# Optimization experiments

Hardware: AMD Instinct MI355X
Metric: run time of the kernel (lower is better)

## Reference

```python
import jax, jax.numpy as jnp
import numpy as np

BLANK = 36
NEG = -1e30  # stand-in for -inf that stays NaN-free under logaddexp


def _ctc_loss(logits, targets, input_lengths, target_lengths):
    """CTC loss (reduction='mean', matching torch.nn.CTCLoss semantics:
    per-sample loss divided by target_length, then mean over batch).
    logits: [B, T, C] raw scores; targets: [B*L] flattened labels (fixed L per sample).
    """
    B, T, C = logits.shape
    L = targets.shape[0] // B
    tgt = targets.reshape(B, L)
    S = 2 * L + 1  # extended label length: blank-interleaved

    # log_softmax over classes, then time-major [T, B, C]
    lp = jnp.transpose(jax.nn.log_softmax(logits, axis=-1), (1, 0, 2))

    # extended targets: [blank, t1, blank, t2, ..., blank]  -> [B, S]
    ext = jnp.full((B, S), BLANK, dtype=tgt.dtype).at[:, 1::2].set(tgt)

    # gather log-probs of extended labels: [T, B, S]
    lp_ext = lp[:, jnp.arange(B)[:, None], ext]

    # positions beyond 2*target_len are invalid
    valid = jnp.arange(S)[None, :] < (2 * target_lengths[:, None] + 1)  # [B, S]
    # skip transition s-2 -> s allowed only if ext[s] != blank and ext[s] != ext[s-2]
    skip_ok = (ext != BLANK) & jnp.concatenate(
        [jnp.zeros((B, 2), bool), ext[:, 2:] != ext[:, :-2]], axis=1)

    end_idx = 2 * target_lengths  # index of final blank; [B]

    def final_ll(alpha):
        e1 = jnp.take_along_axis(alpha, end_idx[:, None], axis=1)[:, 0]
        e2 = jnp.take_along_axis(alpha, (end_idx - 1)[:, None], axis=1)[:, 0]
        return jnp.logaddexp(e1, e2)

    # t = 0 initialization
    alpha0 = jnp.full((B, S), NEG, logits.dtype)
    alpha0 = alpha0.at[:, 0].set(lp_ext[0, :, 0]).at[:, 1].set(lp_ext[0, :, 1])
    alpha0 = jnp.where(valid, alpha0, NEG)
    final0 = jnp.where(input_lengths == 1, final_ll(alpha0), NEG)

    pad1 = jnp.full((B, 1), NEG, logits.dtype)
    pad2 = jnp.full((B, 2), NEG, logits.dtype)

    def step(carry, inp):
        alpha, final = carry
        t, lpe = inp  # lpe: [B, S]
        a1 = jnp.concatenate([pad1, alpha[:, :-1]], axis=1)
        a2 = jnp.where(skip_ok, jnp.concatenate([pad2, alpha[:, :-2]], axis=1), NEG)
        new = jnp.logaddexp(jnp.logaddexp(alpha, a1), a2) + lpe
        new = jnp.where(valid, new, NEG)
        final = jnp.where(input_lengths == t + 1, final_ll(new), final)
        return (new, final), None

    (_, final), _ = jax.lax.scan(step, (alpha0, final0),
                                 (jnp.arange(1, T), lp_ext[1:]))
    return jnp.mean(-final / target_lengths.astype(logits.dtype))


def setup_inputs() -> dict:
    key = jax.random.key(0)
    k1, k2 = jax.random.split(key)
    B, T, C, L = 2048, 256, 37, 16
    logits = jax.random.normal(k1, (B, T, C), dtype=jnp.float32)
    targets = jax.random.randint(k2, (B * L,), 0, 36, dtype=jnp.int32)  # never blank
    input_lengths = jnp.full((B,), T, dtype=jnp.int32)
    target_lengths = jnp.full((B,), L, dtype=jnp.int32)
    return {"logits": logits, "targets": targets,
            "input_lengths": input_lengths, "target_lengths": target_lengths}


def reference(logits, targets, input_lengths, target_lengths):
    return _ctc_loss(logits, targets, input_lengths, target_lengths)
```

## Files before the change

kernel.cpp:

```cpp
#include <hip/hip_runtime.h>

#define BLANK 36
#define NEG -1e30f
#define CC 37
#define LOG37 3.6109179126442243f

__device__ __forceinline__ float logaddexp_f(float a, float b) {
    float m = fmaxf(a, b);
    float d = fabsf(a - b);
    return m + __logf(1.0f + __expf(-d));
}

#define DPP0(src, ctrl) __builtin_amdgcn_update_dpp(0, (src), (ctrl), 0xf, 0xf, true)
#define DPPM(old, src, ctrl) __builtin_amdgcn_update_dpp((old), (src), (ctrl), 0xf, 0xf, false)

__global__ __launch_bounds__(128) void ctc_fused_dpp16_kernel(
    const float* __restrict__ logits,
    const int*   __restrict__ targets,
    const int*   __restrict__ input_lengths,
    const int*   __restrict__ target_lengths,
    float*       __restrict__ per_sample,
    int B, int T, int L)
{
    __shared__ float lds[2 * 4736];
    const int lane = threadIdx.x & 63;
    const int wib  = threadIdx.x >> 6;
    const int b    = blockIdx.x * 2 + wib;
    if (b >= B) return;

    float* X0 = lds + wib * 4736;
    float* X1 = X0 + 2368;

    const int S = 2 * L + 1;
    const int tlen_s = __builtin_amdgcn_readfirstlane(target_lengths[b]);
    const int ilen_s = __builtin_amdgcn_readfirstlane(input_lengths[b]);
    const int end_s  = 2 * tlen_s;

    int ext_s = BLANK;
    if (lane < S && (lane & 1)) ext_s = targets[b * L + (lane >> 1)];
    const int es2 = __shfl_up(ext_s, 2);
    const bool skip_ok = (lane < S) && (lane >= 2) && (ext_s != BLANK) && (ext_s != es2);
    const float kf = skip_ok ? 1.0f : 0.0f;
    const bool valid = lane < (2 * tlen_s + 1);
    const float validm = valid ? 1.0f : 0.0f;

    const bool c16 = ((lane & 31) == 16);
    const bool c17 = ((lane & 31) == 17);
    const bool c32 = (lane == 32);
    const bool c33 = (lane == 33);

    const float4* src = (const float4*)(logits + (size_t)b * T * CC);

    float z = 0.0f, racc = 0.0f, capv = NEG;

    auto STEP = [&](float p, int tt) {
        const int zi  = __float_as_int(z);
        const int s1  = DPP0(zi, 0x111);
        const int s2  = DPP0(zi, 0x112);
        const int b15 = DPP0(zi, 0x142);
        const int b31 = DPP0(zi, 0x143);
        const int y15 = DPP0(s1, 0x142);
        const int y31 = DPP0(s1, 0x143);
        const float a1 = __int_as_float(c16 ? b15 : (c32 ? b31 : s1));
        const float a2 = __int_as_float(c16 ? y15 : (c17 ? b15 : (c32 ? y31 : (c33 ? b31 : s2))));
        z = fmaf(kf, a2, z + a1) * p;
        if (ilen_s == tt + 1)
            capv = __logf(fmaxf(z, 1e-35f)) + racc - (float)(tt + 1) * LOG37;
    };

    auto RESCALE = [&]() {
        float m = z;
        m = fmaxf(m, __int_as_float(DPPM(__float_as_int(m), __float_as_int(m), 0x111)));
        m = fmaxf(m, __int_as_float(DPPM(__float_as_int(m), __float_as_int(m), 0x112)));
        m = fmaxf(m, __int_as_float(DPPM(__float_as_int(m), __float_as_int(m), 0x114)));
        m = fmaxf(m, __int_as_float(DPPM(__float_as_int(m), __float_as_int(m), 0x118)));
        m = fmaxf(m, __int_as_float(DPPM(__float_as_int(m), __float_as_int(m), 0x142)));
        m = fmaxf(m, __int_as_float(DPPM(__float_as_int(m), __float_as_int(m), 0x143)));
        float gm = __int_as_float(__builtin_amdgcn_readlane(__float_as_int(m), 63));
        gm = fmaxf(gm, 1e-30f);
        z *= (1.0f / gm);
        racc += __logf(gm);
    };

    auto SOFTMAX = [&](float* Xn) {
        float xr[CC];
        const float* row = Xn + lane * CC;
        #pragma unroll
        for (int c2 = 0; c2 < CC; ++c2) xr[c2] = row[c2];
        float m = xr[0];
        #pragma unroll
        for (int c2 = 1; c2 < CC; ++c2) m = fmaxf(m, xr[c2]);
        float ss = 0.0f;
        #pragma unroll
        for (int c2 = 0; c2 < CC; ++c2) { xr[c2] = __expf(xr[c2] - m); ss += xr[c2]; }
        const float inv = 37.0f / ss;
        float* wrow = Xn + lane * CC;
        #pragma unroll
        for (int c2 = 0; c2 < CC; ++c2) wrow[c2] = xr[c2] * inv;
    };

    {
        float4* dst = (float4*)X0;
        #pragma unroll
        for (int k = 0; k < 9; ++k) dst[k * 64 + lane] = src[k * 64 + lane];
        if (lane < 16) dst[576 + lane] = src[576 + lane];
        __builtin_amdgcn_s_waitcnt(0);
        SOFTMAX(X0);
        __builtin_amdgcn_s_waitcnt(0);
    }

    const int NC = T >> 6;
    float pw[16];
    #pragma unroll 1
    for (int c = 0; c < NC; ++c) {
        const float* Xb = (c & 1) ? X1 : X0;
        const bool more = (c + 1 < NC);
        const bool first = (c == 0);
        const int tbase = c << 6;

        float4 f0 = {}, f1 = {}, f2 = {}, f3 = {}, f4 = {},
               f5 = {}, f6 = {}, f7 = {}, f8 = {}, f9 = {};
        if (more) {
            const float4* s2g = src + (size_t)(c + 1) * 592;
            f0 = s2g[lane];       f1 = s2g[64 + lane];  f2 = s2g[128 + lane];
            f3 = s2g[192 + lane]; f4 = s2g[256 + lane]; f5 = s2g[320 + lane];
            f6 = s2g[384 + lane]; f7 = s2g[448 + lane]; f8 = s2g[512 + lane];
            if (lane < 16) f9 = s2g[576 + lane];
        }

        #pragma unroll
        for (int j = 0; j < 16; ++j) pw[j] = Xb[j * CC + ext_s];
        #pragma unroll
        for (int r = 0; r < 64; ++r) {
            const float p = pw[r & 15];
            if (r + 16 < 64) pw[r & 15] = Xb[(r + 16) * CC + ext_s];
            if (r == 0) {
                if (first) {
                    z = ((lane <= 1) ? p : 0.0f) * validm;
                    if (ilen_s == 1) capv = __logf(fmaxf(z, 1e-35f)) - LOG37;
                } else {
                    STEP(p, tbase);
                }
            } else {
                STEP(p, tbase + r);
            }
            if ((r & 15) == 15) RESCALE();
        }

        if (more) {
            float* Xn = (c & 1) ? X0 : X1;
            float4* dst = (float4*)Xn;
            dst[lane] = f0;       dst[64 + lane] = f1;  dst[128 + lane] = f2;
            dst[192 + lane] = f3; dst[256 + lane] = f4; dst[320 + lane] = f5;
            dst[384 + lane] = f6; dst[448 + lane] = f7; dst[512 + lane] = f8;
            if (lane < 16) dst[576 + lane] = f9;
            __builtin_amdgcn_s_waitcnt(0);
            SOFTMAX(Xn);
            __builtin_amdgcn_s_waitcnt(0);
        }
    }

    const float e1 = __shfl(capv, end_s);
    const float e2 = __shfl(capv, end_s - 1);
    const float final_v = logaddexp_f(e1, e2);
    if (lane == 0) per_sample[b] = -final_v / (float)tlen_s;
}

__global__ __launch_bounds__(256) void lse_kernel(
    const float* __restrict__ logits, float* __restrict__ denom, int N)
{
    __shared__ float lds[256 * CC];
    const int lane = threadIdx.x & 63;
    const int wib  = threadIdx.x >> 6;
    const int wave = blockIdx.x * 4 + wib;
    const long long row0 = (long long)wave * 64;
    if (row0 >= N) return;
    const int wbase = wib * 64 * CC;
    const float4* src4 = (const float4*)(logits + row0 * CC);
    const long long n4_remaining = ((long long)N * CC - row0 * CC) / 4;
    float4* lds4 = (float4*)(lds + wbase);
    #pragma unroll
    for (int k = 0; k < 10; ++k) {
        const int idx = k * 64 + lane;
        if (idx < 592 && idx < n4_remaining) lds4[idx] = src4[idx];
    }
    __builtin_amdgcn_s_waitcnt(0);
    const long long row = row0 + lane;
    if (row >= N) return;
    const float* x = lds + wbase + lane * CC;
    float m = x[0];
    #pragma unroll
    for (int c = 1; c < CC; ++c) m = fmaxf(m, x[c]);
    float s = 0.0f;
    #pragma unroll
    for (int c = 0; c < CC; ++c) s += __expf(x[c] - m);
    denom[row] = m + __logf(s);
}

__global__ __launch_bounds__(256) void ctc_alpha2_kernel(
    const float* __restrict__ logits, const float* __restrict__ denom,
    const int* __restrict__ targets, const int* __restrict__ input_lengths,
    const int* __restrict__ target_lengths, float* __restrict__ per_sample,
    int B, int T, int L)
{
    const int wave = (int)((blockIdx.x * blockDim.x + threadIdx.x) >> 6);
    const int lane = threadIdx.x & 63;
    if (wave >= B) return;
    const int b = wave;
    const int S = 2 * L + 1;
    const int tlen = target_lengths[b];
    const int ilen = input_lengths[b];
    const int end_idx = 2 * tlen;
    int ext_s = BLANK;
    if (lane < S && (lane & 1)) ext_s = targets[b * L + (lane >> 1)];
    const int ext_sm2 = __shfl_up(ext_s, 2);
    const bool skip_ok = (lane < S) && (lane >= 2) && (ext_s != BLANK) && (ext_s != ext_sm2);
    const bool valid = lane < (2 * tlen + 1);
    const float* lg = logits + (size_t)b * T * CC;
    const float* dn = denom + (size_t)b * T;
    float x_cur = lg[ext_s];
    float d_cur = dn[0];
    float x_nx = (T > 1) ? lg[CC + ext_s] : 0.0f;
    float d_nx = (T > 1) ? dn[1] : 0.0f;
    float final_v = NEG;
    float alpha = (valid && lane <= 1) ? (x_cur - d_cur) : NEG;
    if (ilen == 1) {
        const float e1 = __shfl(alpha, end_idx);
        const float e2 = __shfl(alpha, end_idx - 1);
        final_v = logaddexp_f(e1, e2);
    }
    for (int tt = 1; tt < T; ++tt) {
        x_cur = x_nx; d_cur = d_nx;
        if (tt + 1 < T) {
            x_nx = lg[(size_t)(tt + 1) * CC + ext_s];
            d_nx = dn[tt + 1];
        }
        const float lpe = x_cur - d_cur;
        float a1 = __shfl_up(alpha, 1);
        if (lane == 0) a1 = NEG;
        float a2 = __shfl_up(alpha, 2);
        if (!skip_ok) a2 = NEG;
        const float m = fmaxf(fmaxf(alpha, a1), a2);
        const float s = __expf(alpha - m) + __expf(a1 - m) + __expf(a2 - m);
        const float na = m + __logf(s) + lpe;
        alpha = valid ? na : NEG;
        if (ilen == tt + 1) {
            const float e1 = __shfl(alpha, end_idx);
            const float e2 = __shfl(alpha, end_idx - 1);
            final_v = logaddexp_f(e1, e2);
        }
    }
    if (lane == 0) per_sample[b] = -final_v / (float)tlen;
}

__global__ __launch_bounds__(256) void ctc_alpha_mono_kernel(
    const float* __restrict__ logits, const int* __restrict__ targets,
    const int* __restrict__ input_lengths, const int* __restrict__ target_lengths,
    float* __restrict__ per_sample, int B, int T, int L)
{
    const int wave = (int)((blockIdx.x * blockDim.x + threadIdx.x) >> 6);
    const int lane = threadIdx.x & 63;
    if (wave >= B) return;
    const int b = wave;
    const int S = 2 * L + 1;
    const int tlen = target_lengths[b];
    const int ilen = input_lengths[b];
    const int end_idx = 2 * tlen;
    int ext_s = BLANK;
    if (lane < S && (lane & 1)) ext_s = targets[b * L + (lane >> 1)];
    const int ext_sm2 = __shfl_up(ext_s, 2);
    const bool skip_ok = (lane < S) && (lane >= 2) && (ext_s != BLANK) && (ext_s != ext_sm2);
    const bool valid = lane < (2 * tlen + 1);
    const float* lg = logits + (size_t)b * T * CC;
    float alpha = NEG, final_v = NEG;
    for (int t = 0; t < T; ++t) {
        float x = (lane < CC) ? lg[t * CC + lane] : -3.0e38f;
        float mx = x;
        #pragma unroll
        for (int o = 32; o > 0; o >>= 1) mx = fmaxf(mx, __shfl_xor(mx, o));
        float e = (lane < CC) ? __expf(x - mx) : 0.0f;
        float se = e;
        #pragma unroll
        for (int o = 32; o > 0; o >>= 1) se += __shfl_xor(se, o);
        const float lp = x - mx - __logf(se);
        const float lpe = __shfl(lp, ext_s);
        float newa;
        if (t == 0) {
            newa = (lane <= 1) ? lpe : NEG;
        } else {
            float a1 = __shfl_up(alpha, 1);
            if (lane == 0) a1 = NEG;
            float a2 = __shfl_up(alpha, 2);
            if (!skip_ok) a2 = NEG;
            newa = logaddexp_f(logaddexp_f(alpha, a1), a2) + lpe;
        }
        if (!valid) newa = NEG;
        alpha = newa;
        if (ilen == t + 1) {
            const float e1 = __shfl(alpha, end_idx);
            const float e2 = __shfl(alpha, end_idx - 1);
            final_v = logaddexp_f(e1, e2);
        }
    }
    if (lane == 0) per_sample[b] = -final_v / (float)tlen;
}

__global__ __launch_bounds__(256) void reduce_mean_kernel(
    const float* __restrict__ ps, float* __restrict__ out, int B)
{
    float s = 0.0f;
    for (int i = threadIdx.x; i < B; i += 256) s += ps[i];
    #pragma unroll
    for (int o = 32; o > 0; o >>= 1) s += __shfl_xor(s, o);
    __shared__ float sm[4];
    const int w = threadIdx.x >> 6, l = threadIdx.x & 63;
    if (l == 0) sm[w] = s;
    __syncthreads();
    if (threadIdx.x == 0) {
        out[0] = (sm[0] + sm[1] + sm[2] + sm[3]) / (float)B;
    }
}

extern "C" void kernel_launch(void* const* d_in, const int* in_sizes, int n_in,
                              void* d_out, int out_size, void* d_ws, size_t ws_size,
                              hipStream_t stream) {
    const float* logits         = (const float*)d_in[0];
    const int*   targets        = (const int*)d_in[1];
    const int*   input_lengths  = (const int*)d_in[2];
    const int*   target_lengths = (const int*)d_in[3];

    const int B = in_sizes[2];
    const int L = in_sizes[1] / B;
    const int T = in_sizes[0] / (B * CC);
    const long long N = (long long)B * T;

    float* per_sample = (float*)d_ws;
    float* scratch    = per_sample + B;
    float* out        = (float*)d_out;

    const size_t ws_mid = ((size_t)B + (size_t)N) * sizeof(float);
    const int nblocks_alpha = (B * 64 + 255) / 256;
    const long long nwaves = (N + 63) / 64;

    if ((T % 64 == 0) && T >= 64 && L <= 31 && ws_size >= (size_t)B * sizeof(float)) {
        ctc_fused_dpp16_kernel<<<(B + 1) / 2, 128, 0, stream>>>(
            logits, targets, input_lengths, target_lengths, per_sample, B, T, L);
    } else if (ws_size >= ws_mid && T >= 2) {
        lse_kernel<<<(int)((nwaves + 3) / 4), 256, 0, stream>>>(logits, scratch, (int)N);
        ctc_alpha2_kernel<<<nblocks_alpha, 256, 0, stream>>>(
            logits, scratch, targets, input_lengths, target_lengths, per_sample, B, T, L);
    } else {
        ctc_alpha_mono_kernel<<<nblocks_alpha, 256, 0, stream>>>(
            logits, targets, input_lengths, target_lengths, per_sample, B, T, L);
    }
    reduce_mean_kernel<<<1, 256, 0, stream>>>(per_sample, out, B);
}
```

Baseline: 138.5 us.

## Split CTC recursion into forward-alpha and backward-beta waves per sample

Each block now handles one sample with two waves. One wave runs the forward alpha recursion over the first half of time while the other runs a backward beta recursion from the end over the second half. The two meet in the middle and combine through an LDS exchange and a wave reduction, which halves the serial dependency chain per sample. The cost is twice as many blocks and a midpoint dot-product combine. Single-buffered LDS per wave means loads are no longer double-buffered. The split also assumes ilen > T/2 for the combine path and lacks valid-mask handling in the forward init.

After: 135.3 us. -2.3%, faster.

```diff
diff --git a/kernel.cpp b/kernel.cpp
--- a/kernel.cpp
+++ b/kernel.cpp
@@ -14,7 +14,7 @@
 #define DPP0(src, ctrl) __builtin_amdgcn_update_dpp(0, (src), (ctrl), 0xf, 0xf, true)
 #define DPPM(old, src, ctrl) __builtin_amdgcn_update_dpp((old), (src), (ctrl), 0xf, 0xf, false)
 
-__global__ __launch_bounds__(128) void ctc_fused_dpp16_kernel(
+__global__ __launch_bounds__(128, 4) void ctc_fused_ab_kernel(
     const float* __restrict__ logits,
     const int*   __restrict__ targets,
     const int*   __restrict__ input_lengths,
@@ -22,27 +22,31 @@
     float*       __restrict__ per_sample,
     int B, int T, int L)
 {
-    __shared__ float lds[2 * 4736];
+    __shared__ float lds[2 * 2368 + 66];
     const int lane = threadIdx.x & 63;
     const int wib  = threadIdx.x >> 6;
-    const int b    = blockIdx.x * 2 + wib;
-    if (b >= B) return;
-
-    float* X0 = lds + wib * 4736;
-    float* X1 = X0 + 2368;
+    const int b    = blockIdx.x;
+
+    float* Xw   = lds + wib * 2368;
+    float* exch = lds + 4736;
 
     const int S = 2 * L + 1;
     const int tlen_s = __builtin_amdgcn_readfirstlane(target_lengths[b]);
     const int ilen_s = __builtin_amdgcn_readfirstlane(input_lengths[b]);
     const int end_s  = 2 * tlen_s;
-
-    int ext_s = BLANK;
-    if (lane < S && (lane & 1)) ext_s = targets[b * L + (lane >> 1)];
-    const int es2 = __shfl_up(ext_s, 2);
-    const bool skip_ok = (lane < S) && (lane >= 2) && (ext_s != BLANK) && (ext_s != es2);
-    const float kf = skip_ok ? 1.0f : 0.0f;
-    const bool valid = lane < (2 * tlen_s + 1);
-    const float validm = valid ? 1.0f : 0.0f;
+    const int halfT  = T >> 1;
+    const int NC     = T >> 6;
+    const int NCh    = NC >> 1;
+
+    const int st = (wib == 0) ? lane : (63 - lane);
+    int ext_w = BLANK;
+    if (st < S && (st & 1)) ext_w = targets[b * L + (st >> 1)];
+    const int exo = __shfl_up(ext_w, 2);
+    float kf;
+    if (wib == 0)
+        kf = ((st >= 2) && (st < S) && (ext_w != BLANK) && (ext_w != exo)) ? 1.0f : 0.0f;
+    else
+        kf = ((st + 2 < S) && (exo != BLANK) && (exo != ext_w)) ? 1.0f : 0.0f;
 
     const bool c16 = ((lane & 31) == 16);
     const bool c17 = ((lane & 31) == 17);
@@ -51,25 +55,20 @@
 
     const float4* src = (const float4*)(logits + (size_t)b * T * CC);
 
-    float z = 0.0f, racc = 0.0f, capv = NEG;
-
-    auto STEP = [&](float p, int tt) {
-        const int zi  = __float_as_int(z);
-        const int s1  = DPP0(zi, 0x111);
-        const int s2  = DPP0(zi, 0x112);
-        const int b15 = DPP0(zi, 0x142);
-        const int b31 = DPP0(zi, 0x143);
+    auto SHIFTS = [&](float x, float& a1, float& a2) {
+        const int xi  = __float_as_int(x);
+        const int s1  = DPP0(xi, 0x111);
+        const int s2  = DPP0(xi, 0x112);
+        const int b15 = DPP0(xi, 0x142);
+        const int b31 = DPP0(xi, 0x143);
         const int y15 = DPP0(s1, 0x142);
         const int y31 = DPP0(s1, 0x143);
-        const float a1 = __int_as_float(c16 ? b15 : (c32 ? b31 : s1));
-        const float a2 = __int_as_float(c16 ? y15 : (c17 ? b15 : (c32 ? y31 : (c33 ? b31 : s2))));
-        z = fmaf(kf, a2, z + a1) * p;
-        if (ilen_s == tt + 1)
-            capv = __logf(fmaxf(z, 1e-35f)) + racc - (float)(tt + 1) * LOG37;
+        a1 = __int_as_float(c16 ? b15 : (c32 ? b31 : s1));
+        a2 = __int_as_float(c16 ? y15 : (c17 ? b15 : (c32 ? y31 : (c33 ? b31 : s2))));
     };
 
-    auto RESCALE = [&]() {
-        float m = z;
+    auto RESCALE = [&](float& x, float& racc) {
+        float m = x;
         m = fmaxf(m, __int_as_float(DPPM(__float_as_int(m), __float_as_int(m), 0x111)));
         m = fmaxf(m, __int_as_float(DPPM(__float_as_int(m), __float_as_int(m), 0x112)));
         m = fmaxf(m, __int_as_float(DPPM(__float_as_int(m), __float_as_int(m), 0x114)));
@@ -78,7 +77,7 @@
         m = fmaxf(m, __int_as_float(DPPM(__float_as_int(m), __float_as_int(m), 0x143)));
         float gm = __int_as_float(__builtin_amdgcn_readlane(__float_as_int(m), 63));
         gm = fmaxf(gm, 1e-30f);
-        z *= (1.0f / gm);
+        x *= (1.0f / gm);
         racc += __logf(gm);
     };
 
@@ -99,71 +98,134 @@
         for (int c2 = 0; c2 < CC; ++c2) wrow[c2] = xr[c2] * inv;
     };
 
-    {
-        float4* dst = (float4*)X0;
-        #pragma unroll
-        for (int k = 0; k < 9; ++k) dst[k * 64 + lane] = src[k * 64 + lane];
-        if (lane < 16) dst[576 + lane] = src[576 + lane];
+    auto STAGE = [&](const float4* s2g) {
+        float4* dst = (float4*)Xw;
+        #pragma unroll
+        for (int k = 0; k < 9; ++k) dst[k * 64 + lane] = s2g[k * 64 + lane];
+        if (lane < 16) dst[576 + lane] = s2g[576 + lane];
         __builtin_amdgcn_s_waitcnt(0);
-        SOFTMAX(X0);
+    };
+
+    float z = 0.0f, racc = 0.0f, capv = NEG;
+    float pw[16];
+
+    if (wib == 0) {
+        STAGE(src);
+        SOFTMAX(Xw);
         __builtin_amdgcn_s_waitcnt(0);
-    }
-
-    const int NC = T >> 6;
-    float pw[16];
-    #pragma unroll 1
-    for (int c = 0; c < NC; ++c) {
-        const float* Xb = (c & 1) ? X1 : X0;
-        const bool more = (c + 1 < NC);
-        const bool first = (c == 0);
-        const int tbase = c << 6;
-
-        float4 f0 = {}, f1 = {}, f2 = {}, f3 = {}, f4 = {},
-               f5 = {}, f6 = {}, f7 = {}, f8 = {}, f9 = {};
-        if (more) {
-            const float4* s2g = src + (size_t)(c + 1) * 592;
-            f0 = s2g[lane];       f1 = s2g[64 + lane];  f2 = s2g[128 + lane];
-            f3 = s2g[192 + lane]; f4 = s2g[256 + lane]; f5 = s2g[320 + lane];
-            f6 = s2g[384 + lane]; f7 = s2g[448 + lane]; f8 = s2g[512 + lane];
-            if (lane < 16) f9 = s2g[576 + lane];
-        }
-
-        #pragma unroll
-        for (int j = 0; j < 16; ++j) pw[j] = Xb[j * CC + ext_s];
-        #pragma unroll
-        for (int r = 0; r < 64; ++r) {
-            const float p = pw[r & 15];
-            if (r + 16 < 64) pw[r & 15] = Xb[(r + 16) * CC + ext_s];
-            if (r == 0) {
-                if (first) {
-                    z = ((lane <= 1) ? p : 0.0f) * validm;
+        #pragma unroll 1
+        for (int c = 0; c < NCh; ++c) {
+            const bool more = (c + 1 < NCh);
+            float4 f0 = {}, f1 = {}, f2 = {}, f3 = {}, f4 = {},
+                   f5 = {}, f6 = {}, f7 = {}, f8 = {}, f9 = {};
+            if (more) {
+                const float4* s2g = src + (size_t)(c + 1) * 592;
+                f0 = s2g[lane];       f1 = s2g[64 + lane];  f2 = s2g[128 + lane];
+                f3 = s2g[192 + lane]; f4 = s2g[256 + lane]; f5 = s2g[320 + lane];
+                f6 = s2g[384 + lane]; f7 = s2g[448 + lane]; f8 = s2g[512 + lane];
+                if (lane < 16) f9 = s2g[576 + lane];
+            }
+            const int tbase = c << 6;
+            #pragma unroll
+            for (int j = 0; j < 16; ++j) pw[j] = Xw[j * CC + ext_w];
+            #pragma unroll
+            for (int r = 0; r < 64; ++r) {
+                const float p = pw[r & 15];
+                if (r + 16 < 64) pw[r & 15] = Xw[(r + 16) * CC + ext_w];
+                if (c == 0 && r == 0) {
+                    z = (lane <= 1) ? p : 0.0f;
                     if (ilen_s == 1) capv = __logf(fmaxf(z, 1e-35f)) - LOG37;
                 } else {
-                    STEP(p, tbase);
+                    float a1, a2;
+                    SHIFTS(z, a1, a2);
+                    z = fmaf(kf, a2, z + a1) * p;
+                    const int tt = tbase + r;
+                    if (ilen_s == tt + 1)
+                        capv = __logf(fmaxf(z, 1e-35f)) + racc - (float)(tt + 1) * LOG37;
                 }
-            } else {
-                STEP(p, tbase + r);
-            }
-            if ((r & 15) == 15) RESCALE();
-        }
-
-        if (more) {
-            float* Xn = (c & 1) ? X0 : X1;
-            float4* dst = (float4*)Xn;
-            dst[lane] = f0;       dst[64 + lane] = f1;  dst[128 + lane] = f2;
-            dst[192 + lane] = f3; dst[256 + lane] = f4; dst[320 + lane] = f5;
-            dst[384 + lane] = f6; dst[448 + lane] = f7; dst[512 + lane] = f8;
-            if (lane < 16) dst[576 + lane] = f9;
-            __builtin_amdgcn_s_waitcnt(0);
-            SOFTMAX(Xn);
-            __builtin_amdgcn_s_waitcnt(0);
-        }
-    }
-
-    const float e1 = __shfl(capv, end_s);
-    const float e2 = __shfl(capv, end_s - 1);
-    const float final_v = logaddexp_f(e1, e2);
-    if (lane == 0) per_sample[b] = -final_v / (float)tlen_s;
+                if ((r & 15) == 15) RESCALE(z, racc);
+            }
+            if (more) {
+                float4* dst = (float4*)Xw;
+                dst[lane] = f0;       dst[64 + lane] = f1;  dst[128 + lane] = f2;
+                dst[192 + lane] = f3; dst[256 + lane] = f4; dst[320 + lane] = f5;
+                dst[384 + lane] = f6; dst[448 + lane] = f7; dst[512 + lane] = f8;
+                if (lane < 16) dst[576 + lane] = f9;
+                __builtin_amdgcn_s_waitcnt(0);
+                SOFTMAX(Xw);
+                __builtin_amdgcn_s_waitcnt(0);
+            }
+        }
+    } else {
+        STAGE(src + (size_t)(NC - 1) * 592);
+        SOFTMAX(Xw);
+        __builtin_amdgcn_s_waitcnt(0);
+        const int il1 = ilen_s - 1;
+        #pragma unroll 1
+        for (int i = 0; i < NCh; ++i) {
+            const bool more = (i + 1 < NCh);
+            float4 f0 = {}, f1 = {}, f2 = {}, f3 = {}, f4 = {},
+                   f5 = {}, f6 = {}, f7 = {}, f8 = {}, f9 = {};
+            if (more) {
+                const float4* s2g = src + (size_t)(NC - 2 - i) * 592;
+                f0 = s2g[lane];       f1 = s2g[64 + lane];  f2 = s2g[128 + lane];
+                f3 = s2g[192 + lane]; f4 = s2g[256 + lane]; f5 = s2g[320 + lane];
+                f6 = s2g[384 + lane]; f7 = s2g[448 + lane]; f8 = s2g[512 + lane];
+                if (lane < 16) f9 = s2g[576 + lane];
+            }
+            const int cbase = (NC - 1 - i) << 6;
+            #pragma unroll
+            for (int j = 0; j < 16; ++j) pw[j] = Xw[(63 - j) * CC + ext_w];
+            #pragma unroll
+            for (int r = 0; r < 64; ++r) {
+                const int tt = cbase + 63 - r;
+                if (tt == il1) {
+                    z = (lane == 63 - end_s || lane == 64 - end_s) ? 1.0f : 0.0f;
+                    racc = 0.0f;
+                }
+                const float p = pw[r & 15];
+                if (r + 16 < 64) pw[r & 15] = Xw[(63 - (r + 16)) * CC + ext_w];
+                const float u = z * p;
+                float a1, a2;
+                SHIFTS(u, a1, a2);
+                z = fmaf(kf, a2, u + a1);
+                if ((r & 15) == 15) RESCALE(z, racc);
+            }
+            if (more) {
+                float4* dst = (float4*)Xw;
+                dst[lane] = f0;       dst[64 + lane] = f1;  dst[128 + lane] = f2;
+                dst[192 + lane] = f3; dst[256 + lane] = f4; dst[320 + lane] = f5;
+                dst[384 + lane] = f6; dst[448 + lane] = f7; dst[512 + lane] = f8;
+                if (lane < 16) dst[576 + lane] = f9;
+                __builtin_amdgcn_s_waitcnt(0);
+                SOFTMAX(Xw);
+                __builtin_amdgcn_s_waitcnt(0);
+            }
+        }
+    }
+
+    __syncthreads();
+    if (wib == 1) {
+        exch[63 - lane] = z;
+        if (lane == 0) exch[64] = racc;
+    }
+    __syncthreads();
+    if (wib == 0) {
+        const float bs = exch[lane];
+        const float rb = exch[64];
+        float prod = z * bs;
+        #pragma unroll
+        for (int o = 32; o > 0; o >>= 1) prod += __shfl_xor(prod, o);
+        float final_v;
+        if (ilen_s <= halfT) {
+            const float e1 = __shfl(capv, end_s);
+            const float e2 = __shfl(capv, end_s - 1);
+            final_v = logaddexp_f(e1, e2);
+        } else {
+            final_v = __logf(fmaxf(prod, 1e-37f)) + racc + rb - (float)ilen_s * LOG37;
+        }
+        if (lane == 0) per_sample[b] = -final_v / (float)tlen_s;
+    }
 }
 
 __global__ __launch_bounds__(256) void lse_kernel(
@@ -342,8 +404,8 @@
     const int nblocks_alpha = (B * 64 + 255) / 256;
     const long long nwaves = (N + 63) / 64;
 
-    if ((T % 64 == 0) && T >= 64 && L <= 31 && ws_size >= (size_t)B * sizeof(float)) {
-        ctc_fused_dpp16_kernel<<<(B + 1) / 2, 128, 0, stream>>>(
+    if ((T % 128 == 0) && T >= 128 && L <= 31 && ws_size >= (size_t)B * sizeof(float)) {
+        ctc_fused_ab_kernel<<<B, 128, 0, stream>>>(
             logits, targets, input_lengths, target_lengths, per_sample, B, T, L);
     } else if (ws_size >= ws_mid && T >= 2) {
         lse_kernel<<<(int)((nwaves + 3) / 4), 256, 0, stream>>>(logits, scratch, (int)N);
```
